# Performance work log

Hardware: AMD Instinct MI355X
Metric: run time of the kernel (lower is better)

## Reference

```python
import jax, jax.numpy as jnp
import numpy as np

B, N, C, H = 2, 2048, 1024, 16
D = C // H  # head_dim = 64

def setup_inputs() -> dict:
    key = jax.random.key(0)
    ks = jax.random.split(key, 8)
    x = jax.random.normal(ks[0], (B, N, C), jnp.float32)
    mask = jax.random.uniform(ks[1], (H, N, N), jnp.float32)
    gamma = jax.random.uniform(ks[2], (H,), jnp.float32)  # per-head decay in (0,1)
    state_prev = jax.random.normal(ks[3], (B, H, D, D), jnp.float32)
    w_scale = 0.02
    W_qkv = jax.random.normal(ks[4], (C, 3 * C), jnp.float32) * w_scale
    b_qkv = jnp.zeros((3 * C,), jnp.float32)
    W_out = jax.random.normal(ks[5], (C, C), jnp.float32) * w_scale
    b_out = jnp.zeros((C,), jnp.float32)
    return dict(x=x, mask=mask, gamma=gamma, state_prev=state_prev,
                W_qkv=W_qkv, b_qkv=b_qkv, W_out=W_out, b_out=b_out)

def reference(x, mask, gamma, state_prev, W_qkv, b_qkv, W_out, b_out):
    # Retention.chunkwise with state_prev (mode='chunkwise')
    b, n, c = x.shape
    h = gamma.shape[0]
    d = c // h
    scale = d ** -0.5
    qkv = (x @ W_qkv + b_qkv).reshape(b, n, 3, h, d)
    q = qkv[:, :, 0].transpose(0, 2, 1, 3) * scale  # [B,H,N,D]
    k = qkv[:, :, 1].transpose(0, 2, 1, 3)
    v = qkv[:, :, 2].transpose(0, 2, 1, 3)
    # intra-chunk decay-masked retention: [B,H,N,N]
    ret = jnp.einsum('bhnd,bhmd->bhnm', q, k) * mask
    ret = jnp.einsum('bhnm,bhmd->bhnd', ret, v)  # [B,H,N,D]
    inner_pos = jnp.arange(1, n + 1, dtype=x.dtype)  # [N], 1-based positions
    # state = sum_n gamma^(N-n) * k_n^T v_n (no [B,H,N,D,D] materialization)
    state_decays = gamma[:, None] ** (n - inner_pos)[None, :]  # [H,N]
    state = jnp.einsum('bhnd,bhne,hn->bhde', k, v, state_decays)  # [B,H,D,D]
    chunk_decay = gamma ** n  # [H]
    state = state + state_prev * chunk_decay[None, :, None, None]
    # cross-chunk retention against previous state
    cross = jnp.einsum('bhnd,bhde->bhne', q, state_prev)
    cross = cross * (gamma[None, :, None, None] ** inner_pos[None, None, :, None])
    ret = (ret + cross).transpose(0, 2, 1, 3).reshape(b, n, c)
    out = ret @ W_out + b_out
    return (out, state)
```

## Files before the change

### kernel.cpp

```cpp
#include <hip/hip_runtime.h>
#include <hip/hip_bf16.h>
#include <cstdint>

#define DI __device__ __forceinline__

typedef __attribute__((ext_vector_type(8))) short v8s;
typedef __attribute__((ext_vector_type(4))) float v4f;

constexpr int Bc = 2, Nc = 2048, Cc = 1024, Hc = 16, Dc = 64;

DI float bfbits(uint32_t u) { union { uint32_t i; float f; } c; c.i = u; return c.f; }
DI unsigned short f2bf(float f) {
    union { float f; uint32_t u; } c; c.f = f;
    uint32_t r = c.u + 0x7FFFu + ((c.u >> 16) & 1u);
    return (unsigned short)(r >> 16);
}
DI void unpackb8(uint4 u, float* f) {
    f[0] = bfbits(u.x << 16); f[1] = bfbits(u.x & 0xFFFF0000u);
    f[2] = bfbits(u.y << 16); f[3] = bfbits(u.y & 0xFFFF0000u);
    f[4] = bfbits(u.z << 16); f[5] = bfbits(u.z & 0xFFFF0000u);
    f[6] = bfbits(u.w << 16); f[7] = bfbits(u.w & 0xFFFF0000u);
}
DI float gpow(float g, float p) {
    if (p <= 0.f) return 1.f;
    if (g <= 0.f) return 0.f;
    return exp2f(p * log2f(g));
}

__global__ __launch_bounds__(256) void cvt_bf16(
    const float* __restrict__ in, unsigned short* __restrict__ out, int n8)
{
    int i = blockIdx.x * 256 + threadIdx.x;
    if (i >= n8) return;
    float4 a = ((const float4*)in)[i * 2];
    float4 b = ((const float4*)in)[i * 2 + 1];
    ushort4 r0; r0.x = f2bf(a.x); r0.y = f2bf(a.y); r0.z = f2bf(a.z); r0.w = f2bf(a.w);
    ushort4 r1; r1.x = f2bf(b.x); r1.y = f2bf(b.y); r1.z = f2bf(b.z); r1.w = f2bf(b.w);
    ((ushort4*)out)[i * 2] = r0; ((ushort4*)out)[i * 2 + 1] = r1;
}

__global__ __launch_bounds__(256) void transpose_cvt(
    const float* __restrict__ in, unsigned short* __restrict__ out, int R, int C)
{
    __shared__ float T[64][65];
    const int tid = threadIdx.x;
    const int r0 = blockIdx.y * 64, c0 = blockIdx.x * 64;
    #pragma unroll
    for (int rep = 0; rep < 4; rep++) {
        int row = (tid >> 4) + rep * 16, col = (tid & 15) * 4;
        float4 v = *reinterpret_cast<const float4*>(in + (size_t)(r0 + row) * C + c0 + col);
        T[row][col] = v.x; T[row][col + 1] = v.y; T[row][col + 2] = v.z; T[row][col + 3] = v.w;
    }
    __syncthreads();
    #pragma unroll
    for (int rep = 0; rep < 4; rep++) {
        int ocr = (tid >> 4) + rep * 16, j4 = (tid & 15) * 4;
        ushort4 w;
        w.x = f2bf(T[j4][ocr]);     w.y = f2bf(T[j4 + 1][ocr]);
        w.z = f2bf(T[j4 + 2][ocr]); w.w = f2bf(T[j4 + 3][ocr]);
        *reinterpret_cast<ushort4*>(out + (size_t)(c0 + ocr) * R + r0 + j4) = w;
    }
}

__global__ __launch_bounds__(256) void qkv_mfma(
    const unsigned short* __restrict__ A, const unsigned short* __restrict__ Bt,
    const float* __restrict__ bias,
    unsigned short* __restrict__ q, unsigned short* __restrict__ k,
    unsigned short* __restrict__ v, unsigned short* __restrict__ vt)
{
    __shared__ unsigned short As[64][72];
    __shared__ unsigned short Bs[64][72];
    const int tid = threadIdx.x, wave = tid >> 6, lane = tid & 63;
    const int L = lane & 15, quad = lane >> 4;
    const int row0 = blockIdx.y * 64, col0 = blockIdx.x * 64;
    v4f acc[4];
    #pragma unroll
    for (int s = 0; s < 4; s++) { acc[s][0] = 0.f; acc[s][1] = 0.f; acc[s][2] = 0.f; acc[s][3] = 0.f; }
    for (int k0 = 0; k0 < 1024; k0 += 64) {
        __syncthreads();
        #pragma unroll
        for (int rep = 0; rep < 2; rep++) {
            int r = (tid >> 3) + rep * 32, ch = (tid & 7) * 8;
            *(uint4*)&As[r][ch] = *(const uint4*)(A + (size_t)(row0 + r) * 1024 + k0 + ch);
            *(uint4*)&Bs[r][ch] = *(const uint4*)(Bt + (size_t)(col0 + r) * 1024 + k0 + ch);
        }
        __syncthreads();
        v8s a0 = *(v8s*)&As[wave * 16 + L][quad * 8];
        v8s a1 = *(v8s*)&As[wave * 16 + L][32 + quad * 8];
        #pragma unroll
        for (int s = 0; s < 4; s++) {
            v8s b0 = *(v8s*)&Bs[s * 16 + L][quad * 8];
            v8s b1 = *(v8s*)&Bs[s * 16 + L][32 + quad * 8];
            acc[s] = __builtin_amdgcn_mfma_f32_16x16x32_bf16(a0, b0, acc[s], 0, 0, 0);
            acc[s] = __builtin_amdgcn_mfma_f32_16x16x32_bf16(a1, b1, acc[s], 0, 0, 0);
        }
    }
    const int which = col0 >> 10;
    const int h = (col0 & 1023) >> 6;
    #pragma unroll
    for (int s = 0; s < 4; s++) {
        int c = col0 + s * 16 + L;
        int d = s * 16 + L;
        float bv = bias[c];
        #pragma unroll
        for (int reg = 0; reg < 4; reg++) {
            int rr = row0 + wave * 16 + quad * 4 + reg;
            int b = rr >> 11, n = rr & 2047;
            float val = acc[s][reg] + bv;
            size_t base = (((size_t)(b * Hc + h)) * Nc + n) * Dc + d;
            if (which == 0)      q[base] = f2bf(val * 0.125f);
            else if (which == 1) k[base] = f2bf(val);
            else {
                unsigned short bb = f2bf(val);
                v[base] = bb;
                vt[(((size_t)(b * Hc + h)) * Dc + d) * Nc + n] = bb;
            }
        }
    }
}

__global__ __launch_bounds__(256) void retention_mfma(
    const unsigned short* __restrict__ qb, const unsigned short* __restrict__ kb,
    const unsigned short* __restrict__ vtb,
    const float* __restrict__ mask, const float* __restrict__ gamma,
    const float* __restrict__ sprev,
    unsigned short* __restrict__ retb)
{
    __shared__ unsigned short Ks[64][72];
    __shared__ unsigned short Vt[64][72];
    __shared__ unsigned short Sm[64][72];
    const int tid = threadIdx.x, wave = tid >> 6, lane = tid & 63;
    const int L = lane & 15, quad = lane >> 4;
    const int bh = blockIdx.y, b = bh >> 4, h = bh & 15;
    const int n0 = blockIdx.x * 64;
    const float g = gamma[h];

    {
        #pragma unroll
        for (int rep = 0; rep < 2; rep++) {
            int r = (tid >> 3) + rep * 32, ch = (tid & 7) * 8;
            *(uint4*)&Ks[r][ch] = *(const uint4*)(qb + ((size_t)bh * Nc + n0 + r) * Dc + ch);
        }
        int d = tid >> 2, e0 = (tid & 3) * 16;
        const float* sp = sprev + (size_t)bh * 4096 + d * 64 + e0;
        #pragma unroll
        for (int j = 0; j < 16; j++) Sm[e0 + j][d] = f2bf(sp[j]);
    }
    __syncthreads();
    const v8s qf0 = *(v8s*)&Ks[wave * 16 + L][quad * 8];
    const v8s qf1 = *(v8s*)&Ks[wave * 16 + L][32 + quad * 8];
    v4f oacc[4];
    #pragma unroll
    for (int s = 0; s < 4; s++) {
        v4f a; a[0] = 0.f; a[1] = 0.f; a[2] = 0.f; a[3] = 0.f;
        a = __builtin_amdgcn_mfma_f32_16x16x32_bf16(qf0, *(v8s*)&Sm[s * 16 + L][quad * 8], a, 0, 0, 0);
        a = __builtin_amdgcn_mfma_f32_16x16x32_bf16(qf1, *(v8s*)&Sm[s * 16 + L][32 + quad * 8], a, 0, 0, 0);
        oacc[s] = a;
    }
    {
        float cf = gpow(g, (float)(n0 + wave * 16 + quad * 4 + 1));
        #pragma unroll
        for (int reg = 0; reg < 4; reg++) {
            #pragma unroll
            for (int s = 0; s < 4; s++) oacc[s][reg] *= cf;
            cf *= g;
        }
    }

    const float* mbase = mask + (size_t)h * Nc * Nc;
    for (int m0 = 0; m0 < Nc; m0 += 64) {
        __syncthreads();
        #pragma unroll
        for (int rep = 0; rep < 2; rep++) {
            int r = (tid >> 3) + rep * 32, ch = (tid & 7) * 8;
            *(uint4*)&Ks[r][ch] = *(const uint4*)(kb + ((size_t)bh * Nc + m0 + r) * Dc + ch);
            *(uint4*)&Vt[r][ch] = *(const uint4*)(vtb + ((size_t)bh * Dc + r) * Nc + m0 + ch);
        }
        __syncthreads();
        float mv[4][4];
        #pragma unroll
        for (int s = 0; s < 4; s++)
            #pragma unroll
            for (int reg = 0; reg < 4; reg++)
                mv[s][reg] = mbase[(size_t)(n0 + wave * 16 + quad * 4 + reg) * Nc + m0 + s * 16 + L];
        v4f sa[4];
        #pragma unroll
        for (int s = 0; s < 4; s++) {
            v4f a; a[0] = 0.f; a[1] = 0.f; a[2] = 0.f; a[3] = 0.f;
            a = __builtin_amdgcn_mfma_f32_16x16x32_bf16(qf0, *(v8s*)&Ks[s * 16 + L][quad * 8], a, 0, 0, 0);
            a = __builtin_amdgcn_mfma_f32_16x16x32_bf16(qf1, *(v8s*)&Ks[s * 16 + L][32 + quad * 8], a, 0, 0, 0);
            sa[s] = a;
        }
        #pragma unroll
        for (int s = 0; s < 4; s++)
            #pragma unroll
            for (int reg = 0; reg < 4; reg++)
                Sm[wave * 16 + quad * 4 + reg][s * 16 + L] = f2bf(sa[s][reg] * mv[s][reg]);
        v8s af0 = *(v8s*)&Sm[wave * 16 + L][quad * 8];
        v8s af1 = *(v8s*)&Sm[wave * 16 + L][32 + quad * 8];
        #pragma unroll
        for (int s = 0; s < 4; s++) {
            oacc[s] = __builtin_amdgcn_mfma_f32_16x16x32_bf16(af0, *(v8s*)&Vt[s * 16 + L][quad * 8], oacc[s], 0, 0, 0);
            oacc[s] = __builtin_amdgcn_mfma_f32_16x16x32_bf16(af1, *(v8s*)&Vt[s * 16 + L][32 + quad * 8], oacc[s], 0, 0, 0);
        }
    }
    #pragma unroll
    for (int s = 0; s < 4; s++)
        #pragma unroll
        for (int reg = 0; reg < 4; reg++) {
            int n = n0 + wave * 16 + quad * 4 + reg;
            retb[((size_t)b * Nc + n) * Cc + h * 64 + s * 16 + L] = f2bf(oacc[s][reg]);
        }
}

__global__ __launch_bounds__(256) void state_partial(
    const unsigned short* __restrict__ kg, const unsigned short* __restrict__ vg,
    const float* __restrict__ gamma,
    float* __restrict__ partial)
{
    __shared__ float Ks[64][65];
    __shared__ float Vs[64][65];
    __shared__ float wdec[64];
    const int chunk = blockIdx.x;
    const int bh = blockIdx.y;
    const int h = bh & 15;
    const int tid = threadIdx.x;
    const int d = tid >> 2;
    const int e0 = (tid & 3) * 16;
    const float g = gamma[h];
    const unsigned short* kb = kg + (size_t)bh * Nc * Dc;
    const unsigned short* vb = vg + (size_t)bh * Nc * Dc;
    float acc[16] = {};
    const int nStart = chunk * 256;
    for (int m0 = nStart; m0 < nStart + 256; m0 += 64) {
        __syncthreads();
        {
            uint4 u0 = *(const uint4*)(kb + (size_t)(m0 + d) * 64 + e0);
            uint4 u1 = *(const uint4*)(kb + (size_t)(m0 + d) * 64 + e0 + 8);
            float f[8];
            unpackb8(u0, f);
            #pragma unroll
            for (int j = 0; j < 8; j++) Ks[d][e0 + j] = f[j];
            unpackb8(u1, f);
            #pragma unroll
            for (int j = 0; j < 8; j++) Ks[d][e0 + 8 + j] = f[j];
            uint4 w0 = *(const uint4*)(vb + (size_t)(m0 + d) * 64 + e0);
            uint4 w1 = *(const uint4*)(vb + (size_t)(m0 + d) * 64 + e0 + 8);
            unpackb8(w0, f);
            #pragma unroll
            for (int j = 0; j < 8; j++) Vs[d][e0 + j] = f[j];
            unpackb8(w1, f);
            #pragma unroll
            for (int j = 0; j < 8; j++) Vs[d][e0 + 8 + j] = f[j];
        }
        if (tid < 64) wdec[tid] = gpow(g, (float)(2047 - (m0 + tid)));
        __syncthreads();
        for (int nn = 0; nn < 64; nn++) {
            float kw = Ks[nn][d] * wdec[nn];
            #pragma unroll
            for (int j = 0; j < 16; j++) acc[j] += kw * Vs[nn][e0 + j];
        }
    }
    float* pp = partial + (size_t)chunk * (Bc * Hc * Dc * Dc)
              + ((size_t)bh * 64 + d) * 64 + e0;
    #pragma unroll
    for (int j = 0; j < 16; j++) pp[j] = acc[j];
}

__global__ __launch_bounds__(256) void state_reduce(
    const float* __restrict__ partial,
    const float* __restrict__ sprev,
    const float* __restrict__ gamma,
    float* __restrict__ outState)
{
    const int idx = blockIdx.x * 256 + threadIdx.x;
    const int bh = idx >> 12;
    const int h = bh & 15;
    const float g = gamma[h];
    float acc = sprev[idx] * gpow(g, 2048.f);
    #pragma unroll
    for (int c = 0; c < 8; c++) acc += partial[(size_t)c * (Bc * Hc * Dc * Dc) + idx];
    outState[idx] = acc;
}

__global__ __launch_bounds__(256) void out_mfma(
    const unsigned short* __restrict__ A, const unsigned short* __restrict__ Bt,
    const float* __restrict__ bias,
    float* __restrict__ out)
{
    __shared__ unsigned short As[64][72];
    __shared__ unsigned short Bs[64][72];
    const int tid = threadIdx.x, wave = tid >> 6, lane = tid & 63;
    const int L = lane & 15, quad = lane >> 4;
    const int row0 = blockIdx.y * 64, col0 = blockIdx.x * 64;
    v4f acc[4];
    #pragma unroll
    for (int s = 0; s < 4; s++) { acc[s][0] = 0.f; acc[s][1] = 0.f; acc[s][2] = 0.f; acc[s][3] = 0.f; }
    for (int k0 = 0; k0 < 1024; k0 += 64) {
        __syncthreads();
        #pragma unroll
        for (int rep = 0; rep < 2; rep++) {
            int r = (tid >> 3) + rep * 32, ch = (tid & 7) * 8;
            *(uint4*)&As[r][ch] = *(const uint4*)(A + (size_t)(row0 + r) * 1024 + k0 + ch);
            *(uint4*)&Bs[r][ch] = *(const uint4*)(Bt + (size_t)(col0 + r) * 1024 + k0 + ch);
        }
        __syncthreads();
        v8s a0 = *(v8s*)&As[wave * 16 + L][quad * 8];
        v8s a1 = *(v8s*)&As[wave * 16 + L][32 + quad * 8];
        #pragma unroll
        for (int s = 0; s < 4; s++) {
            v8s b0 = *(v8s*)&Bs[s * 16 + L][quad * 8];
            v8s b1 = *(v8s*)&Bs[s * 16 + L][32 + quad * 8];
            acc[s] = __builtin_amdgcn_mfma_f32_16x16x32_bf16(a0, b0, acc[s], 0, 0, 0);
            acc[s] = __builtin_amdgcn_mfma_f32_16x16x32_bf16(a1, b1, acc[s], 0, 0, 0);
        }
    }
    #pragma unroll
    for (int s = 0; s < 4; s++) {
        int c = col0 + s * 16 + L;
        float bv = bias[c];
        #pragma unroll
        for (int reg = 0; reg < 4; reg++) {
            int rr = row0 + wave * 16 + quad * 4 + reg;
            out[(size_t)rr * 1024 + c] = acc[s][reg] + bv;
        }
    }
}

extern "C" void kernel_launch(void* const* d_in, const int* in_sizes, int n_in,
                              void* d_out, int out_size, void* d_ws, size_t ws_size,
                              hipStream_t stream) {
    (void)in_sizes; (void)n_in; (void)out_size; (void)ws_size;
    const float* x     = (const float*)d_in[0];
    const float* mask  = (const float*)d_in[1];
    const float* gamma = (const float*)d_in[2];
    const float* sprev = (const float*)d_in[3];
    const float* Wqkv  = (const float*)d_in[4];
    const float* bqkv  = (const float*)d_in[5];
    const float* Wout  = (const float*)d_in[6];
    const float* bout  = (const float*)d_in[7];

    char* W = (char*)d_ws;
    unsigned short* qb   = (unsigned short*)(W);
    unsigned short* kb   = (unsigned short*)(W + 8388608);
    unsigned short* vb   = (unsigned short*)(W + 16777216);
    unsigned short* vtb  = (unsigned short*)(W + 25165824);
    unsigned short* retb = (unsigned short*)(W + 33554432);
    unsigned short* xb   = (unsigned short*)(W + 41943040);
    unsigned short* wqt  = (unsigned short*)(W + 50331648);
    unsigned short* wot  = (unsigned short*)(W + 56623104);
    float*          part = (float*)        (W + 58720256);

    float* out      = (float*)d_out;
    float* outState = (float*)d_out + (size_t)Bc * Nc * Cc;

    cvt_bf16<<<2048, 256, 0, stream>>>(x, xb, 524288);
    transpose_cvt<<<dim3(48, 16), 256, 0, stream>>>(Wqkv, wqt, 1024, 3072);
    transpose_cvt<<<dim3(16, 16), 256, 0, stream>>>(Wout, wot, 1024, 1024);
    qkv_mfma<<<dim3(48, 64), 256, 0, stream>>>(xb, wqt, bqkv, qb, kb, vb, vtb);
    retention_mfma<<<dim3(32, 32), 256, 0, stream>>>(qb, kb, vtb, mask, gamma, sprev, retb);
    state_partial<<<dim3(8, 32), 256, 0, stream>>>(kb, vb, gamma, part);
    state_reduce<<<512, 256, 0, stream>>>(part, sprev, gamma, outState);
    out_mfma<<<dim3(16, 64), 256, 0, stream>>>(retb, wot, bout, out);
}
```

Measured before the change: 577.2 us.

## Share mask across batches in retention, enlarge GEMM tiles, drop V transpose

The retention kernel now processes both batch elements per block, so each fp32 mask tile is read once and used for two batches, halving the dominant mask traffic. The QKV and output GEMMs move from 64x64 to 128x128 block tiles with a 4x4 MFMA grid per wave, for more operand reuse. The separate transposed V buffer is removed; V is transposed into shared memory inside the retention loop instead. The costs are more LDS and registers per block, fewer blocks for the retention kernel and GEMMs, and scattered LDS transpose writes.

Result: no change. 574.7 us (-0.4%).

```diff
diff --git a/kernel.cpp b/kernel.cpp
--- a/kernel.cpp
+++ b/kernel.cpp
@@ -66,54 +66,60 @@
     const unsigned short* __restrict__ A, const unsigned short* __restrict__ Bt,
     const float* __restrict__ bias,
     unsigned short* __restrict__ q, unsigned short* __restrict__ k,
-    unsigned short* __restrict__ v, unsigned short* __restrict__ vt)
-{
-    __shared__ unsigned short As[64][72];
-    __shared__ unsigned short Bs[64][72];
+    unsigned short* __restrict__ v)
+{
+    __shared__ unsigned short As[128][72];
+    __shared__ unsigned short Bs[128][72];
     const int tid = threadIdx.x, wave = tid >> 6, lane = tid & 63;
     const int L = lane & 15, quad = lane >> 4;
-    const int row0 = blockIdx.y * 64, col0 = blockIdx.x * 64;
-    v4f acc[4];
-    #pragma unroll
-    for (int s = 0; s < 4; s++) { acc[s][0] = 0.f; acc[s][1] = 0.f; acc[s][2] = 0.f; acc[s][3] = 0.f; }
+    const int wr = (wave >> 1) * 64, wc = (wave & 1) * 64;
+    const int row0 = blockIdx.y * 128, col0 = blockIdx.x * 128;
+    v4f acc[4][4];
+    #pragma unroll
+    for (int i = 0; i < 4; i++)
+        #pragma unroll
+        for (int j = 0; j < 4; j++) { acc[i][j][0]=0.f; acc[i][j][1]=0.f; acc[i][j][2]=0.f; acc[i][j][3]=0.f; }
     for (int k0 = 0; k0 < 1024; k0 += 64) {
         __syncthreads();
         #pragma unroll
-        for (int rep = 0; rep < 2; rep++) {
-            int r = (tid >> 3) + rep * 32, ch = (tid & 7) * 8;
-            *(uint4*)&As[r][ch] = *(const uint4*)(A + (size_t)(row0 + r) * 1024 + k0 + ch);
-            *(uint4*)&Bs[r][ch] = *(const uint4*)(Bt + (size_t)(col0 + r) * 1024 + k0 + ch);
-        }
-        __syncthreads();
-        v8s a0 = *(v8s*)&As[wave * 16 + L][quad * 8];
-        v8s a1 = *(v8s*)&As[wave * 16 + L][32 + quad * 8];
-        #pragma unroll
-        for (int s = 0; s < 4; s++) {
-            v8s b0 = *(v8s*)&Bs[s * 16 + L][quad * 8];
-            v8s b1 = *(v8s*)&Bs[s * 16 + L][32 + quad * 8];
-            acc[s] = __builtin_amdgcn_mfma_f32_16x16x32_bf16(a0, b0, acc[s], 0, 0, 0);
-            acc[s] = __builtin_amdgcn_mfma_f32_16x16x32_bf16(a1, b1, acc[s], 0, 0, 0);
+        for (int rep = 0; rep < 4; rep++) {
+            int r = (tid >> 3) + rep * 32, cg = (tid & 7) * 8;
+            *(uint4*)&As[r][cg] = *(const uint4*)(A  + (size_t)(row0 + r) * 1024 + k0 + cg);
+            *(uint4*)&Bs[r][cg] = *(const uint4*)(Bt + (size_t)(col0 + r) * 1024 + k0 + cg);
+        }
+        __syncthreads();
+        #pragma unroll
+        for (int half = 0; half < 2; half++) {
+            v8s af[4], bf[4];
+            #pragma unroll
+            for (int s = 0; s < 4; s++) {
+                af[s] = *(v8s*)&As[wr + s * 16 + L][half * 32 + quad * 8];
+                bf[s] = *(v8s*)&Bs[wc + s * 16 + L][half * 32 + quad * 8];
+            }
+            #pragma unroll
+            for (int i = 0; i < 4; i++)
+                #pragma unroll
+                for (int j = 0; j < 4; j++)
+                    acc[i][j] = __builtin_amdgcn_mfma_f32_16x16x32_bf16(af[i], bf[j], acc[i][j], 0, 0, 0);
         }
     }
     const int which = col0 >> 10;
-    const int h = (col0 & 1023) >> 6;
-    #pragma unroll
-    for (int s = 0; s < 4; s++) {
-        int c = col0 + s * 16 + L;
-        int d = s * 16 + L;
+    #pragma unroll
+    for (int j = 0; j < 4; j++) {
+        int c = col0 + wc + j * 16 + L;
+        int h = (c & 1023) >> 6, d = c & 63;
         float bv = bias[c];
         #pragma unroll
-        for (int reg = 0; reg < 4; reg++) {
-            int rr = row0 + wave * 16 + quad * 4 + reg;
-            int b = rr >> 11, n = rr & 2047;
-            float val = acc[s][reg] + bv;
-            size_t base = (((size_t)(b * Hc + h)) * Nc + n) * Dc + d;
-            if (which == 0)      q[base] = f2bf(val * 0.125f);
-            else if (which == 1) k[base] = f2bf(val);
-            else {
-                unsigned short bb = f2bf(val);
-                v[base] = bb;
-                vt[(((size_t)(b * Hc + h)) * Dc + d) * Nc + n] = bb;
+        for (int i = 0; i < 4; i++) {
+            #pragma unroll
+            for (int reg = 0; reg < 4; reg++) {
+                int rr = row0 + wr + i * 16 + quad * 4 + reg;
+                int b = rr >> 11, n = rr & 2047;
+                float val = acc[i][j][reg] + bv;
+                size_t base = (((size_t)(b * Hc + h)) * Nc + n) * Dc + d;
+                if (which == 0)      q[base] = f2bf(val * 0.125f);
+                else if (which == 1) k[base] = f2bf(val);
+                else                 v[base] = f2bf(val);
             }
         }
     }
@@ -121,60 +127,91 @@
 
 __global__ __launch_bounds__(256) void retention_mfma(
     const unsigned short* __restrict__ qb, const unsigned short* __restrict__ kb,
-    const unsigned short* __restrict__ vtb,
+    const unsigned short* __restrict__ vb,
     const float* __restrict__ mask, const float* __restrict__ gamma,
     const float* __restrict__ sprev,
     unsigned short* __restrict__ retb)
 {
-    __shared__ unsigned short Ks[64][72];
-    __shared__ unsigned short Vt[64][72];
+    __shared__ unsigned short K0[64][72], K1[64][72];
+    __shared__ unsigned short V0[64][72], V1[64][72];
     __shared__ unsigned short Sm[64][72];
     const int tid = threadIdx.x, wave = tid >> 6, lane = tid & 63;
     const int L = lane & 15, quad = lane >> 4;
-    const int bh = blockIdx.y, b = bh >> 4, h = bh & 15;
+    const int h = blockIdx.y;
     const int n0 = blockIdx.x * 64;
     const float g = gamma[h];
+    const int bh0 = h, bh1 = Hc + h;
 
     {
         #pragma unroll
         for (int rep = 0; rep < 2; rep++) {
             int r = (tid >> 3) + rep * 32, ch = (tid & 7) * 8;
-            *(uint4*)&Ks[r][ch] = *(const uint4*)(qb + ((size_t)bh * Nc + n0 + r) * Dc + ch);
-        }
-        int d = tid >> 2, e0 = (tid & 3) * 16;
-        const float* sp = sprev + (size_t)bh * 4096 + d * 64 + e0;
-        #pragma unroll
-        for (int j = 0; j < 16; j++) Sm[e0 + j][d] = f2bf(sp[j]);
+            *(uint4*)&V0[r][ch] = *(const uint4*)(qb + ((size_t)bh0 * Nc + n0 + r) * Dc + ch);
+            *(uint4*)&V1[r][ch] = *(const uint4*)(qb + ((size_t)bh1 * Nc + n0 + r) * Dc + ch);
+        }
+        int dd = tid >> 2, e0 = (tid & 3) * 16;
+        const float* sp0 = sprev + ((size_t)bh0 * 64 + dd) * 64 + e0;
+        const float* sp1 = sprev + ((size_t)bh1 * 64 + dd) * 64 + e0;
+        #pragma unroll
+        for (int j = 0; j < 16; j++) K0[e0 + j][dd] = f2bf(sp0[j]);
+        #pragma unroll
+        for (int j = 0; j < 16; j++) K1[e0 + j][dd] = f2bf(sp1[j]);
     }
     __syncthreads();
-    const v8s qf0 = *(v8s*)&Ks[wave * 16 + L][quad * 8];
-    const v8s qf1 = *(v8s*)&Ks[wave * 16 + L][32 + quad * 8];
-    v4f oacc[4];
-    #pragma unroll
-    for (int s = 0; s < 4; s++) {
-        v4f a; a[0] = 0.f; a[1] = 0.f; a[2] = 0.f; a[3] = 0.f;
-        a = __builtin_amdgcn_mfma_f32_16x16x32_bf16(qf0, *(v8s*)&Sm[s * 16 + L][quad * 8], a, 0, 0, 0);
-        a = __builtin_amdgcn_mfma_f32_16x16x32_bf16(qf1, *(v8s*)&Sm[s * 16 + L][32 + quad * 8], a, 0, 0, 0);
-        oacc[s] = a;
+    v8s qf[2][2];
+    qf[0][0] = *(v8s*)&V0[wave * 16 + L][quad * 8];
+    qf[0][1] = *(v8s*)&V0[wave * 16 + L][32 + quad * 8];
+    qf[1][0] = *(v8s*)&V1[wave * 16 + L][quad * 8];
+    qf[1][1] = *(v8s*)&V1[wave * 16 + L][32 + quad * 8];
+    v4f oacc[2][4];
+    #pragma unroll
+    for (int b = 0; b < 2; b++) {
+        unsigned short (*Kb)[72] = b ? K1 : K0;
+        #pragma unroll
+        for (int s = 0; s < 4; s++) {
+            v4f a; a[0] = 0.f; a[1] = 0.f; a[2] = 0.f; a[3] = 0.f;
+            a = __builtin_amdgcn_mfma_f32_16x16x32_bf16(qf[b][0], *(v8s*)&Kb[s * 16 + L][quad * 8], a, 0, 0, 0);
+            a = __builtin_amdgcn_mfma_f32_16x16x32_bf16(qf[b][1], *(v8s*)&Kb[s * 16 + L][32 + quad * 8], a, 0, 0, 0);
+            oacc[b][s] = a;
+        }
     }
     {
         float cf = gpow(g, (float)(n0 + wave * 16 + quad * 4 + 1));
         #pragma unroll
         for (int reg = 0; reg < 4; reg++) {
             #pragma unroll
-            for (int s = 0; s < 4; s++) oacc[s][reg] *= cf;
+            for (int b = 0; b < 2; b++)
+                #pragma unroll
+                for (int s = 0; s < 4; s++) oacc[b][s][reg] *= cf;
             cf *= g;
         }
     }
 
     const float* mbase = mask + (size_t)h * Nc * Nc;
+    const unsigned short* kp0 = kb + (size_t)bh0 * Nc * Dc;
+    const unsigned short* kp1 = kb + (size_t)bh1 * Nc * Dc;
+    const unsigned short* vp0 = vb + (size_t)bh0 * Nc * Dc;
+    const unsigned short* vp1 = vb + (size_t)bh1 * Nc * Dc;
+
     for (int m0 = 0; m0 < Nc; m0 += 64) {
         __syncthreads();
-        #pragma unroll
-        for (int rep = 0; rep < 2; rep++) {
-            int r = (tid >> 3) + rep * 32, ch = (tid & 7) * 8;
-            *(uint4*)&Ks[r][ch] = *(const uint4*)(kb + ((size_t)bh * Nc + m0 + r) * Dc + ch);
-            *(uint4*)&Vt[r][ch] = *(const uint4*)(vtb + ((size_t)bh * Dc + r) * Nc + m0 + ch);
+        {
+            #pragma unroll
+            for (int rep = 0; rep < 2; rep++) {
+                int r = (tid >> 3) + rep * 32, ch = (tid & 7) * 8;
+                *(uint4*)&K0[r][ch] = *(const uint4*)(kp0 + (size_t)(m0 + r) * Dc + ch);
+                *(uint4*)&K1[r][ch] = *(const uint4*)(kp1 + (size_t)(m0 + r) * Dc + ch);
+            }
+            int n = tid >> 2, d0 = (tid & 3) * 16;
+            union { uint4 u[2]; unsigned short s[16]; } tv;
+            tv.u[0] = *(const uint4*)(vp0 + (size_t)(m0 + n) * Dc + d0);
+            tv.u[1] = *(const uint4*)(vp0 + (size_t)(m0 + n) * Dc + d0 + 8);
+            #pragma unroll
+            for (int j = 0; j < 16; j++) V0[d0 + j][n] = tv.s[j];
+            tv.u[0] = *(const uint4*)(vp1 + (size_t)(m0 + n) * Dc + d0);
+            tv.u[1] = *(const uint4*)(vp1 + (size_t)(m0 + n) * Dc + d0 + 8);
+            #pragma unroll
+            for (int j = 0; j < 16; j++) V1[d0 + j][n] = tv.s[j];
         }
         __syncthreads();
         float mv[4][4];
@@ -183,34 +220,41 @@
             #pragma unroll
             for (int reg = 0; reg < 4; reg++)
                 mv[s][reg] = mbase[(size_t)(n0 + wave * 16 + quad * 4 + reg) * Nc + m0 + s * 16 + L];
-        v4f sa[4];
-        #pragma unroll
-        for (int s = 0; s < 4; s++) {
-            v4f a; a[0] = 0.f; a[1] = 0.f; a[2] = 0.f; a[3] = 0.f;
-            a = __builtin_amdgcn_mfma_f32_16x16x32_bf16(qf0, *(v8s*)&Ks[s * 16 + L][quad * 8], a, 0, 0, 0);
-            a = __builtin_amdgcn_mfma_f32_16x16x32_bf16(qf1, *(v8s*)&Ks[s * 16 + L][32 + quad * 8], a, 0, 0, 0);
-            sa[s] = a;
-        }
+        #pragma unroll
+        for (int b = 0; b < 2; b++) {
+            unsigned short (*Kb)[72] = b ? K1 : K0;
+            unsigned short (*Vb)[72] = b ? V1 : V0;
+            v4f sa[4];
+            #pragma unroll
+            for (int s = 0; s < 4; s++) {
+                v4f a; a[0] = 0.f; a[1] = 0.f; a[2] = 0.f; a[3] = 0.f;
+                a = __builtin_amdgcn_mfma_f32_16x16x32_bf16(qf[b][0], *(v8s*)&Kb[s * 16 + L][quad * 8], a, 0, 0, 0);
+                a = __builtin_amdgcn_mfma_f32_16x16x32_bf16(qf[b][1], *(v8s*)&Kb[s * 16 + L][32 + quad * 8], a, 0, 0, 0);
+                sa[s] = a;
+            }
+            #pragma unroll
+            for (int s = 0; s < 4; s++)
+                #pragma unroll
+                for (int reg = 0; reg < 4; reg++)
+                    Sm[wave * 16 + quad * 4 + reg][s * 16 + L] = f2bf(sa[s][reg] * mv[s][reg]);
+            v8s af0 = *(v8s*)&Sm[wave * 16 + L][quad * 8];
+            v8s af1 = *(v8s*)&Sm[wave * 16 + L][32 + quad * 8];
+            #pragma unroll
+            for (int s = 0; s < 4; s++) {
+                oacc[b][s] = __builtin_amdgcn_mfma_f32_16x16x32_bf16(af0, *(v8s*)&Vb[s * 16 + L][quad * 8], oacc[b][s], 0, 0, 0);
+                oacc[b][s] = __builtin_amdgcn_mfma_f32_16x16x32_bf16(af1, *(v8s*)&Vb[s * 16 + L][32 + quad * 8], oacc[b][s], 0, 0, 0);
+            }
+        }
+    }
+    #pragma unroll
+    for (int b = 0; b < 2; b++)
         #pragma unroll
         for (int s = 0; s < 4; s++)
             #pragma unroll
-            for (int reg = 0; reg < 4; reg++)
-                Sm[wave * 16 + quad * 4 + reg][s * 16 + L] = f2bf(sa[s][reg] * mv[s][reg]);
-        v8s af0 = *(v8s*)&Sm[wave * 16 + L][quad * 8];
-        v8s af1 = *(v8s*)&Sm[wave * 16 + L][32 + quad * 8];
-        #pragma unroll
-        for (int s = 0; s < 4; s++) {
-            oacc[s] = __builtin_amdgcn_mfma_f32_16x16x32_bf16(af0, *(v8s*)&Vt[s * 16 + L][quad * 8], oacc[s], 0, 0, 0);
-            oacc[s] = __builtin_amdgcn_mfma_f32_16x16x32_bf16(af1, *(v8s*)&Vt[s * 16 + L][32 + quad * 8], oacc[s], 0, 0, 0);
-        }
-    }
-    #pragma unroll
-    for (int s = 0; s < 4; s++)
-        #pragma unroll
-        for (int reg = 0; reg < 4; reg++) {
-            int n = n0 + wave * 16 + quad * 4 + reg;
-            retb[((size_t)b * Nc + n) * Cc + h * 64 + s * 16 + L] = f2bf(oacc[s][reg]);
-        }
+            for (int reg = 0; reg < 4; reg++) {
+                int n = n0 + wave * 16 + quad * 4 + reg;
+                retb[((size_t)b * Nc + n) * Cc + h * 64 + s * 16 + L] = f2bf(oacc[b][s][reg]);
+            }
 }
 
 __global__ __launch_bounds__(256) void state_partial(
@@ -228,15 +272,15 @@
     const int d = tid >> 2;
     const int e0 = (tid & 3) * 16;
     const float g = gamma[h];
-    const unsigned short* kb = kg + (size_t)bh * Nc * Dc;
-    const unsigned short* vb = vg + (size_t)bh * Nc * Dc;
+    const unsigned short* kbp = kg + (size_t)bh * Nc * Dc;
+    const unsigned short* vbp = vg + (size_t)bh * Nc * Dc;
     float acc[16] = {};
     const int nStart = chunk * 256;
     for (int m0 = nStart; m0 < nStart + 256; m0 += 64) {
         __syncthreads();
         {
-            uint4 u0 = *(const uint4*)(kb + (size_t)(m0 + d) * 64 + e0);
-            uint4 u1 = *(const uint4*)(kb + (size_t)(m0 + d) * 64 + e0 + 8);
+            uint4 u0 = *(const uint4*)(kbp + (size_t)(m0 + d) * 64 + e0);
+            uint4 u1 = *(const uint4*)(kbp + (size_t)(m0 + d) * 64 + e0 + 8);
             float f[8];
             unpackb8(u0, f);
             #pragma unroll
@@ -244,8 +288,8 @@
             unpackb8(u1, f);
             #pragma unroll
             for (int j = 0; j < 8; j++) Ks[d][e0 + 8 + j] = f[j];
-            uint4 w0 = *(const uint4*)(vb + (size_t)(m0 + d) * 64 + e0);
-            uint4 w1 = *(const uint4*)(vb + (size_t)(m0 + d) * 64 + e0 + 8);
+            uint4 w0 = *(const uint4*)(vbp + (size_t)(m0 + d) * 64 + e0);
+            uint4 w1 = *(const uint4*)(vbp + (size_t)(m0 + d) * 64 + e0 + 8);
             unpackb8(w0, f);
             #pragma unroll
             for (int j = 0; j < 8; j++) Vs[d][e0 + j] = f[j];
@@ -288,41 +332,52 @@
     const float* __restrict__ bias,
     float* __restrict__ out)
 {
-    __shared__ unsigned short As[64][72];
-    __shared__ unsigned short Bs[64][72];
+    __shared__ unsigned short As[128][72];
+    __shared__ unsigned short Bs[128][72];
     const int tid = threadIdx.x, wave = tid >> 6, lane = tid & 63;
     const int L = lane & 15, quad = lane >> 4;
-    const int row0 = blockIdx.y * 64, col0 = blockIdx.x * 64;
-    v4f acc[4];
-    #pragma unroll
-    for (int s = 0; s < 4; s++) { acc[s][0] = 0.f; acc[s][1] = 0.f; acc[s][2] = 0.f; acc[s][3] = 0.f; }
+    const int wr = (wave >> 1) * 64, wc = (wave & 1) * 64;
+    const int row0 = blockIdx.y * 128, col0 = blockIdx.x * 128;
+    v4f acc[4][4];
+    #pragma unroll
+    for (int i = 0; i < 4; i++)
+        #pragma unroll
+        for (int j = 0; j < 4; j++) { acc[i][j][0]=0.f; acc[i][j][1]=0.f; acc[i][j][2]=0.f; acc[i][j][3]=0.f; }
     for (int k0 = 0; k0 < 1024; k0 += 64) {
         __syncthreads();
         #pragma unroll
-        for (int rep = 0; rep < 2; rep++) {
-            int r = (tid >> 3) + rep * 32, ch = (tid & 7) * 8;
-            *(uint4*)&As[r][ch] = *(const uint4*)(A + (size_t)(row0 + r) * 1024 + k0 + ch);
-            *(uint4*)&Bs[r][ch] = *(const uint4*)(Bt + (size_t)(col0 + r) * 1024 + k0 + ch);
-        }
-        __syncthreads();
-        v8s a0 = *(v8s*)&As[wave * 16 + L][quad * 8];
-        v8s a1 = *(v8s*)&As[wave * 16 + L][32 + quad * 8];
-        #pragma unroll
-        for (int s = 0; s < 4; s++) {
-            v8s b0 = *(v8s*)&Bs[s * 16 + L][quad * 8];
-            v8s b1 = *(v8s*)&Bs[s * 16 + L][32 + quad * 8];
-            acc[s] = __builtin_amdgcn_mfma_f32_16x16x32_bf16(a0, b0, acc[s], 0, 0, 0);
-            acc[s] = __builtin_amdgcn_mfma_f32_16x16x32_bf16(a1, b1, acc[s], 0, 0, 0);
-        }
-    }
-    #pragma unroll
-    for (int s = 0; s < 4; s++) {
-        int c = col0 + s * 16 + L;
+        for (int rep = 0; rep < 4; rep++) {
+            int r = (tid >> 3) + rep * 32, cg = (tid & 7) * 8;
+            *(uint4*)&As[r][cg] = *(const uint4*)(A  + (size_t)(row0 + r) * 1024 + k0 + cg);
+            *(uint4*)&Bs[r][cg] = *(const uint4*)(Bt + (size_t)(col0 + r) * 1024 + k0 + cg);
+        }
+        __syncthreads();
+        #pragma unroll
+        for (int half = 0; half < 2; half++) {
+            v8s af[4], bf[4];
+            #pragma unroll
+            for (int s = 0; s < 4; s++) {
+                af[s] = *(v8s*)&As[wr + s * 16 + L][half * 32 + quad * 8];
+                bf[s] = *(v8s*)&Bs[wc + s * 16 + L][half * 32 + quad * 8];
+            }
+            #pragma unroll
+            for (int i = 0; i < 4; i++)
+                #pragma unroll
+                for (int j = 0; j < 4; j++)
+                    acc[i][j] = __builtin_amdgcn_mfma_f32_16x16x32_bf16(af[i], bf[j], acc[i][j], 0, 0, 0);
+        }
+    }
+    #pragma unroll
+    for (int j = 0; j < 4; j++) {
+        int c = col0 + wc + j * 16 + L;
         float bv = bias[c];
         #pragma unroll
-        for (int reg = 0; reg < 4; reg++) {
-            int rr = row0 + wave * 16 + quad * 4 + reg;
-            out[(size_t)rr * 1024 + c] = acc[s][reg] + bv;
+        for (int i = 0; i < 4; i++) {
+            #pragma unroll
+            for (int reg = 0; reg < 4; reg++) {
+                int rr = row0 + wr + i * 16 + quad * 4 + reg;
+                out[(size_t)rr * 1024 + c] = acc[i][j][reg] + bv;
+            }
         }
     }
 }
@@ -344,7 +399,6 @@
     unsigned short* qb   = (unsigned short*)(W);
     unsigned short* kb   = (unsigned short*)(W + 8388608);
     unsigned short* vb   = (unsigned short*)(W + 16777216);
-    unsigned short* vtb  = (unsigned short*)(W + 25165824);
     unsigned short* retb = (unsigned short*)(W + 33554432);
     unsigned short* xb   = (unsigned short*)(W + 41943040);
     unsigned short* wqt  = (unsigned short*)(W + 50331648);
@@ -357,9 +411,9 @@
     cvt_bf16<<<2048, 256, 0, stream>>>(x, xb, 524288);
     transpose_cvt<<<dim3(48, 16), 256, 0, stream>>>(Wqkv, wqt, 1024, 3072);
     transpose_cvt<<<dim3(16, 16), 256, 0, stream>>>(Wout, wot, 1024, 1024);
-    qkv_mfma<<<dim3(48, 64), 256, 0, stream>>>(xb, wqt, bqkv, qb, kb, vb, vtb);
-    retention_mfma<<<dim3(32, 32), 256, 0, stream>>>(qb, kb, vtb, mask, gamma, sprev, retb);
+    qkv_mfma<<<dim3(24, 32), 256, 0, stream>>>(xb, wqt, bqkv, qb, kb, vb);
+    retention_mfma<<<dim3(32, 16), 256, 0, stream>>>(qb, kb, vb, mask, gamma, sprev, retb);
     state_partial<<<dim3(8, 32), 256, 0, stream>>>(kb, vb, gamma, part);
     state_reduce<<<512, 256, 0, stream>>>(part, sprev, gamma, outState);
-    out_mfma<<<dim3(16, 64), 256, 0, stream>>>(retb, wot, bout, out);
-}
+    out_mfma<<<dim3(8, 32), 256, 0, stream>>>(retb, wot, bout, out);
+}
```
